# Performance work log

Measured on AMD Instinct MI355X. Metric: run time of the kernel, lower is better.

## Reference

```python
import jax, jax.numpy as jnp
import numpy as np

N_PAIRS = 100000
N_TRIP = 500000
PAIR_DIM = 128
GEOM_DIM = 4


def _mlp(x, w1, b1, w2, b2):
    return jax.nn.silu(x @ w1 + b1) @ w2 + b2


def setup_inputs() -> dict:
    key = jax.random.key(0)
    ks = jax.random.split(key, 16)

    def lin(k, fan_in, fan_out):
        bound = 1.0 / np.sqrt(fan_in)
        kw, kb = jax.random.split(k)
        w = jax.random.uniform(kw, (fan_in, fan_out), jnp.float32, -bound, bound)
        b = jax.random.uniform(kb, (fan_out,), jnp.float32, -bound, bound)
        return w, b

    psi_w1, psi_b1 = lin(ks[0], 3 * PAIR_DIM + GEOM_DIM, PAIR_DIM)
    psi_w2, psi_b2 = lin(ks[1], PAIR_DIM, PAIR_DIM)
    phi_w1, phi_b1 = lin(ks[2], 2 * PAIR_DIM, PAIR_DIM)
    phi_w2, phi_b2 = lin(ks[3], PAIR_DIM, PAIR_DIM)

    return {
        "h_pair": jax.random.normal(ks[4], (N_PAIRS, PAIR_DIM), jnp.float32),
        "pair_vu_idx": jax.random.randint(ks[5], (N_TRIP,), 0, N_PAIRS, jnp.int64 if jax.config.jax_enable_x64 else jnp.int32).astype(jnp.int32),
        "pair_uw_idx": jax.random.randint(ks[6], (N_TRIP,), 0, N_PAIRS).astype(jnp.int32),
        "pair_vw_idx": jax.random.randint(ks[7], (N_TRIP,), 0, N_PAIRS).astype(jnp.int32),
        "geom_features": jax.random.normal(ks[8], (N_TRIP, GEOM_DIM), jnp.float32),
        "psi_w1": psi_w1, "psi_b1": psi_b1, "psi_w2": psi_w2, "psi_b2": psi_b2,
        "phi_w1": phi_w1, "phi_b1": phi_b1, "phi_w2": phi_w2, "phi_b2": phi_b2,
    }


def reference(h_pair, pair_vu_idx, pair_uw_idx, pair_vw_idx, geom_features,
              psi_w1, psi_b1, psi_w2, psi_b2,
              phi_w1, phi_b1, phi_w2, phi_b2):
    # gather triplet endpoints: [T, pair_dim] each
    h_vu = h_pair[pair_vu_idx]
    h_uw = h_pair[pair_uw_idx]
    h_vw = h_pair[pair_vw_idx]
    triplet_input = jnp.concatenate([h_vu, h_uw, h_vw, geom_features], axis=-1)  # [T, 3D+G]
    m_triplet = _mlp(triplet_input, psi_w1, psi_b1, psi_w2, psi_b2)  # [T, D]
    # scatter-add back onto pairs indexed by vw
    agg = jax.ops.segment_sum(m_triplet, pair_vw_idx, num_segments=h_pair.shape[0])  # [N, D]
    updated = _mlp(jnp.concatenate([h_pair, agg], axis=-1), phi_w1, phi_b1, phi_w2, phi_b2)
    return h_pair + updated
```

## Files before the change

kernel.cpp:

```cpp
#include <hip/hip_runtime.h>
#include <hip/hip_bf16.h>

#define T_TRIP 500000
#define NP     100000
#define NTILES 7813
#define NPAD   500032

typedef float f32x4 __attribute__((ext_vector_type(4)));
typedef __bf16 bf16x8 __attribute__((ext_vector_type(8)));
typedef unsigned short u16;
typedef unsigned short u16x8 __attribute__((ext_vector_type(8)));
typedef unsigned int u32;

__device__ __forceinline__ u16 f2bf(float f) {
  union { float f; unsigned u; } v; v.f = f;
  unsigned r = v.u + 0x7fffu + ((v.u >> 16) & 1u);
  return (u16)(r >> 16);
}

__device__ __forceinline__ ushort4 cvt4(float4 v) {
  ushort4 o; o.x = f2bf(v.x); o.y = f2bf(v.y); o.z = f2bf(v.z); o.w = f2bf(v.w);
  return o;
}

__device__ __forceinline__ u16 cvt1_pk(float v) {
  unsigned r;
  asm("v_cvt_pk_bf16_f32 %0, %1, %1" : "=v"(r) : "v"(v));
  return (u16)r;
}

__device__ __forceinline__ float bflo(u32 d) {
  union { u32 u; float f; } v; v.u = d << 16; return v.f;
}
__device__ __forceinline__ float bfhi(u32 d) {
  union { u32 u; float f; } v; v.u = d & 0xffff0000u; return v.f;
}

#define MFMA16(a, b, c) __builtin_amdgcn_mfma_f32_16x16x32_bf16((a), (b), (c), 0, 0, 0)

#define WAITVM(N) asm volatile("s_waitcnt vmcnt(" #N ")" ::: "memory")
#define LGKM0()   asm volatile("s_waitcnt lgkmcnt(0)" ::: "memory")

__device__ __forceinline__ void barrier_raw() {
  asm volatile("" ::: "memory");
  __builtin_amdgcn_s_barrier();
  asm volatile("" ::: "memory");
  __builtin_amdgcn_sched_barrier(0);
}

__device__ __forceinline__ void gload_lds16(const u16* g, u16* l) {
  __builtin_amdgcn_global_load_lds((const __attribute__((address_space(1))) void*)g,
                                   (__attribute__((address_space(3))) void*)l, 16, 0, 0);
}
__device__ __forceinline__ void gload_lds4(const int* g, int* l) {
  __builtin_amdgcn_global_load_lds((const __attribute__((address_space(1))) void*)g,
                                   (__attribute__((address_space(3))) void*)l, 4, 0, 0);
}

#define FP_W1A   0u
#define FP_W1B   16384u
#define FP_W1C   32768u
#define FP_W2    49152u
#define FP_PW1   65536u
#define FP_PW2   98304u
#define FP_W1D   114688u
#define FP_H     131072u
#define FP_AGG   12931072u
#define SB_CNT2    51462144ull
#define SB_CURSOR2 51862144ull
#define SB_BSUM2   52262144ull
#define SB_TRIP    52262656ull
#define WS_S2      60263168ull

#define HSTR   136
#define HSTR2  132
#define GSTR   520
#define X2STR  264

__global__ void k_pre(const float* __restrict__ psi_w1, const float* __restrict__ psi_w2,
                      const float* __restrict__ phi_w1, const float* __restrict__ phi_w2,
                      const float* __restrict__ h, const int* __restrict__ ivw,
                      u16* __restrict__ ws, int* __restrict__ cnt) {
  const int b = blockIdx.x;
  if (b < 450) {
    int i = b * 256 + threadIdx.x;
    if (i < 49152) {
      int s = i / 16384, r = i % 16384;
      int n = r / 128, k = r % 128;
      ws[FP_W1A + i] = f2bf(psi_w1[(s * 128 + k) * 128 + n]);
      return;
    }
    i -= 49152;
    if (i < 16384) {
      int n = i / 128, k = i % 128;
      ws[FP_W2 + i] = f2bf(psi_w2[k * 128 + n]);
      return;
    }
    i -= 16384;
    if (i < 32768) {
      int n = i / 256, k = i % 256;
      ws[FP_PW1 + i] = f2bf(phi_w1[k * 128 + n]);
      return;
    }
    i -= 32768;
    if (i < 16384) {
      int n = i / 128, k = i % 128;
      ws[FP_PW2 + i] = f2bf(phi_w2[k * 128 + n]);
      return;
    }
    i -= 16384;
    if (i < 512) {
      int k = i / 128, n = i % 128;
      reinterpret_cast<float*>(ws + FP_W1D)[i] = psi_w1[(384 + k) * 128 + n];
    }
  } else if (b < 6700) {
    const size_t i = (size_t)((b - 450) * 256 + threadIdx.x) * 8;
    float4 v0 = *reinterpret_cast<const float4*>(h + i);
    float4 v1 = *reinterpret_cast<const float4*>(h + i + 4);
    *reinterpret_cast<ushort4*>(ws + FP_H + i)     = cvt4(v0);
    *reinterpret_cast<ushort4*>(ws + FP_H + i + 4) = cvt4(v1);
    ushort4 z = {0, 0, 0, 0};
    *reinterpret_cast<ushort4*>(ws + FP_AGG + i)     = z;
    *reinterpret_cast<ushort4*>(ws + FP_AGG + i + 4) = z;
  } else {
    int i = (b - 6700) * 256 + threadIdx.x;
    if (i < T_TRIP) atomicAdd(&cnt[ivw[i]], 1);
  }
}

__global__ __launch_bounds__(1024) void k_scan1(const int* __restrict__ cnt,
                                                int* __restrict__ cursor, int* __restrict__ bsum) {
  __shared__ int wsum[16];
  const int idx = blockIdx.x * 1024 + threadIdx.x;
  const int lane = threadIdx.x & 63, wid = threadIdx.x >> 6;
  int v = (idx < NP) ? cnt[idx] : 0;
  int x = v;
#pragma unroll
  for (int off = 1; off < 64; off <<= 1) {
    int n = __shfl_up(x, off);
    if (lane >= off) x += n;
  }
  if (lane == 63) wsum[wid] = x;
  __syncthreads();
  if (threadIdx.x < 16) {
    int s = wsum[threadIdx.x];
#pragma unroll
    for (int off = 1; off < 16; off <<= 1) {
      int n = __shfl_up(s, off);
      if (threadIdx.x >= off) s += n;
    }
    wsum[threadIdx.x] = s;
  }
  __syncthreads();
  const int base = wid ? wsum[wid - 1] : 0;
  if (idx < NP) cursor[idx] = base + x - v;
  if (threadIdx.x == 1023) bsum[blockIdx.x] = base + x;
}

__global__ void k_scan2(int* __restrict__ bsum) {
  __shared__ int s[128];
  const int t = threadIdx.x;
  int v = (t < 98) ? bsum[t] : 0;
  s[t] = v; __syncthreads();
#pragma unroll
  for (int off = 1; off < 128; off <<= 1) {
    int a = (t >= off) ? s[t - off] : 0;
    __syncthreads();
    s[t] += a;
    __syncthreads();
  }
  if (t < 98) bsum[t] = s[t] - v;
}

__global__ void k_scan3(const int* __restrict__ bsum, int* __restrict__ cursor) {
  int idx = blockIdx.x * 256 + threadIdx.x;
  if (idx < NP) cursor[idx] += bsum[idx >> 10];
}

__global__ void k_perm_pack(const int* __restrict__ ivu, const int* __restrict__ iuw,
                            const int* __restrict__ ivw, const float* __restrict__ geom,
                            int* __restrict__ cursor, int4* __restrict__ trip) {
  int i = blockIdx.x * 256 + threadIdx.x;
  if (i < T_TRIP) {
    int v = ivw[i];
    int pos = atomicAdd(&cursor[v], 1);
    float4 g = reinterpret_cast<const float4*>(geom)[i];
    u32 pk0, pk1;
    asm("v_cvt_pk_bf16_f32 %0, %1, %2" : "=v"(pk0) : "v"(g.x), "v"(g.y));
    asm("v_cvt_pk_bf16_f32 %0, %1, %2" : "=v"(pk1) : "v"(g.z), "v"(g.w));
    int4 rec;
    rec.x = ivu[i] | ((v & 0x7fff) << 17);
    rec.y = iuw[i] | ((v >> 15) << 17);
    rec.z = (int)pk0;
    rec.w = (int)pk1;
    trip[pos] = rec;
  } else if (i < NPAD) {
    int4 z = {0, 0, 0, 0};
    trip[i] = z;
  }
}

__global__ __launch_bounds__(256, 3) void k_triplet_sortagg(
    const u16* __restrict__ H, const int* __restrict__ trip,
    const u16* __restrict__ W1A, const u16* __restrict__ W1B, const u16* __restrict__ W1C,
    const float* __restrict__ w1dF, const u16* __restrict__ W2T,
    const float* __restrict__ b1, const float* __restrict__ b2,
    u16* __restrict__ AGG) {
  __shared__ __align__(16) u16 XB[2][16 * GSTR];
  __shared__ __align__(16) u16 hl[64 * HSTR2];
  __shared__ __align__(16) int aosT[2][256];

  u32* mlu = reinterpret_cast<u32*>(hl);

  const int tid = threadIdx.x;
  const int w = tid >> 6, l = tid & 63;
  const int lr = l & 15;
  const int lk = (l >> 4) << 3;
  const int n0 = w * 32 + lr;
  const int rowh = (l >> 4) << 2;
  const int srow = l >> 4;
  const int schunk = (l & 15) ^ ((l >> 4) << 1);

  bf16x8 w2f[4][2];
#pragma unroll
  for (int ks = 0; ks < 4; ++ks)
#pragma unroll
    for (int ct = 0; ct < 2; ++ct)
      w2f[ks][ct] = *reinterpret_cast<const bf16x8*>(&W2T[(size_t)(n0 + ct * 16) * 128 + ks * 32 + lk]);
  const float b1v[2] = {b1[n0], b1[n0 + 16]};
  const float b2v[2] = {b2[n0], b2[n0 + 16]};
  float w1dv[4][2];
#pragma unroll
  for (int k = 0; k < 4; ++k) {
    w1dv[k][0] = w1dF[k * 128 + n0];
    w1dv[k][1] = w1dF[k * 128 + n0 + 16];
  }

  auto get_idx = [&](int cb, int r, int sel) -> int {
    if (sel == 0) return aosT[cb][r * 4] & 0x1FFFF;
    if (sel == 1) return aosT[cb][r * 4 + 1] & 0x1FFFF;
    u32 d0 = (u32)aosT[cb][r * 4], d1 = (u32)aosT[cb][r * 4 + 1];
    return (int)((d0 >> 17) | ((d1 >> 17) << 15));
  };

  auto stage_src = [&](int cb, int sel, int buf) {
#pragma unroll
    for (int q = 0; q < 4; ++q) {
      const int g = w * 4 + q;
      const int idx = get_idx(cb, g * 4 + srow, sel);
      gload_lds16(H + (size_t)idx * 128 + schunk * 8, &XB[buf][g * GSTR]);
    }
  };

  auto stage_aos = [&](int tile, int cb) {
    const int* src = trip + (size_t)tile * 256;
    gload_lds4(src + w * 64 + l, &aosT[cb][w * 64]);
  };

  auto gemm_src = [&](const u16* WT, int buf, f32x4 (&acc)[4][2]) {
#pragma unroll
    for (int ks = 0; ks < 4; ++ks) {
      bf16x8 a[4], b[2];
#pragma unroll
      for (int rt = 0; rt < 4; ++rt) {
        const int r = rt * 16 + lr;
        const int g = r >> 2, s = r & 3;
        const int j = ks * 4 + (l >> 4);
        a[rt] = *reinterpret_cast<const bf16x8*>(&XB[buf][g * GSTR + s * 128 + ((j ^ (s << 1)) << 3)]);
      }
#pragma unroll
      for (int ct = 0; ct < 2; ++ct)
        b[ct] = *reinterpret_cast<const bf16x8*>(&WT[(size_t)(n0 + ct * 16) * 128 + ks * 32 + lk]);
#pragma unroll
      for (int rt = 0; rt < 4; ++rt)
#pragma unroll
        for (int ct = 0; ct < 2; ++ct)
          acc[rt][ct] = MFMA16(a[rt], b[ct], acc[rt][ct]);
    }
  };

  int cur = 0, pb = 0;
  int tt = blockIdx.x;
  const int G = gridDim.x;

  {
    int t1 = tt + G; if (t1 >= NTILES) t1 = NTILES - 1;
    stage_aos(tt, 0);
    stage_aos(t1, 1);
    WAITVM(0);
    barrier_raw();
    stage_src(0, 0 , 0);
  }

  for (; tt < NTILES; tt += G) {
    const int t0 = tt * 64;

    stage_src(cur, 1 , pb ^ 1);
    WAITVM(4);
    barrier_raw();

    f32x4 acc[4][2] = {};
    gemm_src(W1A, pb, acc);
    barrier_raw();

    stage_src(cur, 2 , pb);
    WAITVM(4);
    barrier_raw();

    gemm_src(W1B, pb ^ 1, acc);
    WAITVM(0);
    barrier_raw();

    stage_src(cur ^ 1, 0 , pb ^ 1);
    gemm_src(W1C, pb, acc);

#pragma unroll
    for (int rt = 0; rt < 4; ++rt)
#pragma unroll
      for (int j = 0; j < 4; ++j) {
        const int row = rt * 16 + rowh + j;
        const u32 d2 = (u32)aosT[cur][row * 4 + 2];
        const u32 d3 = (u32)aosT[cur][row * 4 + 3];
        const float gx = bflo(d2), gy = bfhi(d2), gz = bflo(d3), gw = bfhi(d3);
#pragma unroll
        for (int ct = 0; ct < 2; ++ct)
          acc[rt][ct][j] += gx * w1dv[0][ct] + gy * w1dv[1][ct] +
                            gz * w1dv[2][ct] + gw * w1dv[3][ct];
      }
#pragma unroll
    for (int rt = 0; rt < 4; ++rt)
#pragma unroll
      for (int ct = 0; ct < 2; ++ct) {
        const float bb = b1v[ct];
#pragma unroll
        for (int j = 0; j < 4; ++j) {
          float v = acc[rt][ct][j] + bb;
          v = v * __builtin_amdgcn_rcpf(1.f + __expf(-v));
          hl[(rt * 16 + rowh + j) * HSTR2 + n0 + ct * 16] = cvt1_pk(v);
        }
      }
    LGKM0();
    barrier_raw();

    f32x4 acc2[4][2] = {};
#pragma unroll
    for (int ks = 0; ks < 4; ++ks) {
      bf16x8 a[4];
#pragma unroll
      for (int rt = 0; rt < 4; ++rt)
        a[rt] = *reinterpret_cast<const bf16x8*>(&hl[(rt * 16 + lr) * HSTR2 + ks * 32 + lk]);
#pragma unroll
      for (int rt = 0; rt < 4; ++rt)
#pragma unroll
        for (int ct = 0; ct < 2; ++ct)
          acc2[rt][ct] = MFMA16(a[rt], w2f[ks][ct], acc2[rt][ct]);
    }
    barrier_raw();

#pragma unroll
    for (int rt = 0; rt < 4; ++rt)
#pragma unroll
      for (int j = 0; j < 4; ++j) {
        const int row = rt * 16 + rowh + j;
        float v0 = acc2[rt][0][j] + b2v[0];
        float v1 = acc2[rt][1][j] + b2v[1];
        float x0 = __shfl_xor(v0, 1);
        float x1 = __shfl_xor(v1, 1);
        const bool even = (l & 1) == 0;
        float lo = even ? v0 : x1;
        float hi = even ? x0 : v1;
        const int dcol = even ? (n0 >> 1) : ((n0 + 15) >> 1);
        u32 pk;
        asm("v_cvt_pk_bf16_f32 %0, %1, %2" : "=v"(pk) : "v"(lo), "v"(hi));
        mlu[row * 66 + dcol] = pk;
      }
    LGKM0();
    barrier_raw();

    {
      auto get_vw = [&](int r) -> int {
        u32 d0 = (u32)aosT[cur][r * 4], d1 = (u32)aosT[cur][r * 4 + 1];
        return (int)((d0 >> 17) | ((d1 >> 17) << 15));
      };
      float lo = 0.f, hi = 0.f;
      int vwc = get_vw(w * 16);
#pragma unroll 1
      for (int r8 = 0; r8 < 16; ++r8) {
        const int row = w * 16 + r8;
        const u32 d = mlu[row * 66 + l];
        if (t0 + row < T_TRIP) { lo += bflo(d); hi += bfhi(d); }
        const int vwn = (row < 63) ? get_vw(row + 1) : -1;
        if ((r8 == 15) || (vwn != vwc)) {
          u16* p = AGG + (size_t)vwc * 128 + l * 2;
          u32 pk;
          asm("v_cvt_pk_bf16_f32 %0, %1, %2" : "=v"(pk) : "v"(lo), "v"(hi));
          asm volatile("global_atomic_pk_add_bf16 %0, %1, off" :: "v"(p), "v"(pk) : "memory");
          lo = 0.f; hi = 0.f; vwc = vwn;
        }
      }
    }
    barrier_raw();

    {
      int t2 = tt + 2 * G; if (t2 >= NTILES) t2 = NTILES - 1;
      stage_aos(t2, cur);
    }

    WAITVM(0);
    barrier_raw();
    pb ^= 1; cur ^= 1;
  }
  WAITVM(0);
}

__global__ __launch_bounds__(256, 3) void k_pair_fast(
    const float* __restrict__ h_pair, const u16* __restrict__ H, const u16* __restrict__ AGG,
    const u16* __restrict__ PW1T, const u16* __restrict__ PW2T,
    const float* __restrict__ b1, const float* __restrict__ b2,
    float* __restrict__ out) {
  __shared__ __align__(16) u16 xl[64 * X2STR];
  __shared__ __align__(16) u16 hl[64 * HSTR];

  const int tid = threadIdx.x;
  const int r0 = blockIdx.x * 64;

  {
    const int row = tid >> 2, q = tid & 3;
    int rc = r0 + row; rc = (rc < NP) ? rc : (NP - 1);
    const u16x8* sh = reinterpret_cast<const u16x8*>(H + (size_t)rc * 128 + q * 32);
    const u16x8* sa = reinterpret_cast<const u16x8*>(AGG + (size_t)rc * 128 + q * 32);
    u16x8* d1 = reinterpret_cast<u16x8*>(&xl[row * X2STR + q * 32]);
    u16x8* d2 = reinterpret_cast<u16x8*>(&xl[row * X2STR + 128 + q * 32]);
#pragma unroll
    for (int i = 0; i < 4; ++i) { d1[i] = sh[i]; d2[i] = sa[i]; }
  }
  __syncthreads();

  const int w = tid >> 6, l = tid & 63;
  const int lr = l & 15;
  const int lk = (l >> 4) << 3;
  const int n0 = w * 32 + lr;
  const int rowh = (l >> 4) << 2;

  f32x4 acc[4][2] = {};
#pragma unroll 1
  for (int ks = 0; ks < 8; ++ks) {
    const int k0 = ks * 32;
    bf16x8 a[4], b[2];
#pragma unroll
    for (int rt = 0; rt < 4; ++rt)
      a[rt] = *reinterpret_cast<const bf16x8*>(&xl[(rt * 16 + lr) * X2STR + k0 + lk]);
#pragma unroll
    for (int ct = 0; ct < 2; ++ct)
      b[ct] = *reinterpret_cast<const bf16x8*>(&PW1T[(size_t)(n0 + ct * 16) * 256 + k0 + lk]);
#pragma unroll
    for (int rt = 0; rt < 4; ++rt)
#pragma unroll
      for (int ct = 0; ct < 2; ++ct)
        acc[rt][ct] = MFMA16(a[rt], b[ct], acc[rt][ct]);
  }

  {
    const float b1v0 = b1[n0], b1v1 = b1[n0 + 16];
#pragma unroll
    for (int rt = 0; rt < 4; ++rt)
#pragma unroll
      for (int ct = 0; ct < 2; ++ct) {
        const float bb = ct ? b1v1 : b1v0;
#pragma unroll
        for (int j = 0; j < 4; ++j) {
          float v = acc[rt][ct][j] + bb;
          v = v * __builtin_amdgcn_rcpf(1.f + __expf(-v));
          hl[(rt * 16 + rowh + j) * HSTR + n0 + ct * 16] = cvt1_pk(v);
        }
      }
  }
  __syncthreads();

  f32x4 acc2[4][2] = {};
#pragma unroll
  for (int ks = 0; ks < 4; ++ks) {
    const int k0 = ks * 32;
    bf16x8 a[4], b[2];
#pragma unroll
    for (int rt = 0; rt < 4; ++rt)
      a[rt] = *reinterpret_cast<const bf16x8*>(&hl[(rt * 16 + lr) * HSTR + k0 + lk]);
#pragma unroll
    for (int ct = 0; ct < 2; ++ct)
      b[ct] = *reinterpret_cast<const bf16x8*>(&PW2T[(size_t)(n0 + ct * 16) * 128 + k0 + lk]);
#pragma unroll
    for (int rt = 0; rt < 4; ++rt)
#pragma unroll
      for (int ct = 0; ct < 2; ++ct)
        acc2[rt][ct] = MFMA16(a[rt], b[ct], acc2[rt][ct]);
  }

  {
    const float b2v0 = b2[n0], b2v1 = b2[n0 + 16];
#pragma unroll
    for (int rt = 0; rt < 4; ++rt)
#pragma unroll
      for (int j = 0; j < 4; ++j) {
        const int row = rt * 16 + rowh + j;
        const int r = r0 + row;
        if (r < NP) {
          out[(size_t)r * 128 + n0]      = h_pair[(size_t)r * 128 + n0]      + acc2[rt][0][j] + b2v0;
          out[(size_t)r * 128 + n0 + 16] = h_pair[(size_t)r * 128 + n0 + 16] + acc2[rt][1][j] + b2v1;
        }
      }
  }
}

#define PSI_W1T_OFF 0
#define PSI_W2T_OFF 53248
#define PHI_W1T_OFF 69632
#define PHI_W2T_OFF 102400
#define WS_U16_TOTAL 118784
#define XSTR 424

__global__ void k_prep(const float* __restrict__ psi_w1, const float* __restrict__ psi_w2,
                       const float* __restrict__ phi_w1, const float* __restrict__ phi_w2,
                       u16* __restrict__ ws) {
  int i = blockIdx.x * 256 + threadIdx.x;
  if (i < 128 * 416) {
    int n = i / 416, k = i % 416;
    ws[PSI_W1T_OFF + i] = f2bf(k < 388 ? psi_w1[k * 128 + n] : 0.f);
    return;
  }
  i -= 128 * 416;
  if (i < 128 * 128) {
    int n = i / 128, k = i % 128;
    ws[PSI_W2T_OFF + i] = f2bf(psi_w2[k * 128 + n]);
    return;
  }
  i -= 128 * 128;
  if (i < 128 * 256) {
    int n = i / 256, k = i % 256;
    ws[PHI_W1T_OFF + i] = f2bf(phi_w1[k * 128 + n]);
    return;
  }
  i -= 128 * 256;
  if (i < 128 * 128) {
    int n = i / 128, k = i % 128;
    ws[PHI_W2T_OFF + i] = f2bf(phi_w2[k * 128 + n]);
  }
}

__global__ __launch_bounds__(256, 2) void k_triplet(
    const float* __restrict__ h_pair,
    const int* __restrict__ ivu, const int* __restrict__ iuw, const int* __restrict__ ivw,
    const float* __restrict__ geom,
    const u16* __restrict__ W1T, const u16* __restrict__ W2T,
    const float* __restrict__ b1, const float* __restrict__ b2,
    float* __restrict__ agg) {
  __shared__ __align__(16) u16 xl[64 * XSTR];
  __shared__ __align__(16) u16 hl[64 * HSTR];
  __shared__ int svw[64];

  const int tid = threadIdx.x;
  const int t0 = blockIdx.x * 64;

  {
    const int row = tid >> 2, q = tid & 3;
    const int t = t0 + row;
    const int tc = (t < T_TRIP) ? t : (T_TRIP - 1);
    if (q == 0) svw[row] = (t < T_TRIP) ? ivw[tc] : -1;
    int idx[3];
    idx[0] = ivu[tc]; idx[1] = iuw[tc]; idx[2] = ivw[tc];
#pragma unroll
    for (int s = 0; s < 3; ++s) {
      const float4* src = reinterpret_cast<const float4*>(h_pair + (size_t)idx[s] * 128 + q * 32);
      u16* dst = &xl[row * XSTR + s * 128 + q * 32];
#pragma unroll
      for (int i = 0; i < 8; ++i)
        *reinterpret_cast<ushort4*>(dst + i * 4) = cvt4(src[i]);
    }
  }
  if (tid < 64) {
    const int t = t0 + tid;
    const int tc = (t < T_TRIP) ? t : (T_TRIP - 1);
    const float4 g = reinterpret_cast<const float4*>(geom)[tc];
    u16* dst = &xl[tid * XSTR + 384];
    *reinterpret_cast<ushort4*>(dst) = cvt4(g);
    ushort4 z = {0, 0, 0, 0};
#pragma unroll
    for (int i = 1; i < 8; ++i) *reinterpret_cast<ushort4*>(dst + i * 4) = z;
  }
  __syncthreads();

  const int w = tid >> 6;
  const int l = tid & 63;
  const int lr = l & 15;
  const int lk = (l >> 4) << 3;
  const int n0 = w * 32 + lr;
  const int rowh = (l >> 4) << 2;

  f32x4 acc[4][2] = {};
#pragma unroll 1
  for (int ks = 0; ks < 13; ++ks) {
    const int k0 = ks * 32;
    bf16x8 a[4], b[2];
#pragma unroll
    for (int rt = 0; rt < 4; ++rt)
      a[rt] = *reinterpret_cast<const bf16x8*>(&xl[(rt * 16 + lr) * XSTR + k0 + lk]);
#pragma unroll
    for (int ct = 0; ct < 2; ++ct)
      b[ct] = *reinterpret_cast<const bf16x8*>(&W1T[(size_t)(n0 + ct * 16) * 416 + k0 + lk]);
#pragma unroll
    for (int rt = 0; rt < 4; ++rt)
#pragma unroll
      for (int ct = 0; ct < 2; ++ct)
        acc[rt][ct] = MFMA16(a[rt], b[ct], acc[rt][ct]);
  }

  {
    const float b1v0 = b1[n0], b1v1 = b1[n0 + 16];
#pragma unroll
    for (int rt = 0; rt < 4; ++rt)
#pragma unroll
      for (int ct = 0; ct < 2; ++ct) {
        const float bb = ct ? b1v1 : b1v0;
#pragma unroll
        for (int j = 0; j < 4; ++j) {
          float v = acc[rt][ct][j] + bb;
          v = v / (1.f + __expf(-v));
          hl[(rt * 16 + rowh + j) * HSTR + n0 + ct * 16] = f2bf(v);
        }
      }
  }
  __syncthreads();

  f32x4 acc2[4][2] = {};
#pragma unroll
  for (int ks = 0; ks < 4; ++ks) {
    const int k0 = ks * 32;
    bf16x8 a[4], b[2];
#pragma unroll
    for (int rt = 0; rt < 4; ++rt)
      a[rt] = *reinterpret_cast<const bf16x8*>(&hl[(rt * 16 + lr) * HSTR + k0 + lk]);
#pragma unroll
    for (int ct = 0; ct < 2; ++ct)
      b[ct] = *reinterpret_cast<const bf16x8*>(&W2T[(size_t)(n0 + ct * 16) * 128 + k0 + lk]);
#pragma unroll
    for (int rt = 0; rt < 4; ++rt)
#pragma unroll
      for (int ct = 0; ct < 2; ++ct)
        acc2[rt][ct] = MFMA16(a[rt], b[ct], acc2[rt][ct]);
  }

  {
    const float b2v0 = b2[n0], b2v1 = b2[n0 + 16];
#pragma unroll
    for (int rt = 0; rt < 4; ++rt)
#pragma unroll
      for (int j = 0; j < 4; ++j) {
        const int row = rt * 16 + rowh + j;
        const int dst = svw[row];
        if (dst >= 0) {
          unsafeAtomicAdd(&agg[(size_t)dst * 128 + n0], acc2[rt][0][j] + b2v0);
          unsafeAtomicAdd(&agg[(size_t)dst * 128 + n0 + 16], acc2[rt][1][j] + b2v1);
        }
      }
  }
}

__global__ __launch_bounds__(256, 2) void k_pair(
    const float* __restrict__ h_pair,
    const u16* __restrict__ W1T, const u16* __restrict__ W2T,
    const float* __restrict__ b1, const float* __restrict__ b2,
    float* __restrict__ out) {
  __shared__ __align__(16) u16 xl[64 * X2STR];
  __shared__ __align__(16) u16 hl[64 * HSTR];

  const int tid = threadIdx.x;
  const int r0 = blockIdx.x * 64;

  {
    const int row = tid >> 2, q = tid & 3;
    const int r = r0 + row;
    const int rc = (r < NP) ? r : (NP - 1);
    const float4* s1 = reinterpret_cast<const float4*>(h_pair + (size_t)rc * 128 + q * 32);
    const float4* s2 = reinterpret_cast<const float4*>(out + (size_t)rc * 128 + q * 32);
    u16* d1 = &xl[row * X2STR + q * 32];
    u16* d2 = &xl[row * X2STR + 128 + q * 32];
#pragma unroll
    for (int i = 0; i < 8; ++i) {
      *reinterpret_cast<ushort4*>(d1 + i * 4) = cvt4(s1[i]);
      *reinterpret_cast<ushort4*>(d2 + i * 4) = cvt4(s2[i]);
    }
  }
  __syncthreads();

  const int w = tid >> 6;
  const int l = tid & 63;
  const int lr = l & 15;
  const int lk = (l >> 4) << 3;
  const int n0 = w * 32 + lr;
  const int rowh = (l >> 4) << 2;

  f32x4 acc[4][2] = {};
#pragma unroll 1
  for (int ks = 0; ks < 8; ++ks) {
    const int k0 = ks * 32;
    bf16x8 a[4], b[2];
#pragma unroll
    for (int rt = 0; rt < 4; ++rt)
      a[rt] = *reinterpret_cast<const bf16x8*>(&xl[(rt * 16 + lr) * X2STR + k0 + lk]);
#pragma unroll
    for (int ct = 0; ct < 2; ++ct)
      b[ct] = *reinterpret_cast<const bf16x8*>(&W1T[(size_t)(n0 + ct * 16) * 256 + k0 + lk]);
#pragma unroll
    for (int rt = 0; rt < 4; ++rt)
#pragma unroll
      for (int ct = 0; ct < 2; ++ct)
        acc[rt][ct] = MFMA16(a[rt], b[ct], acc[rt][ct]);
  }

  {
    const float b1v0 = b1[n0], b1v1 = b1[n0 + 16];
#pragma unroll
    for (int rt = 0; rt < 4; ++rt)
#pragma unroll
      for (int ct = 0; ct < 2; ++ct) {
        const float bb = ct ? b1v1 : b1v0;
#pragma unroll
        for (int j = 0; j < 4; ++j) {
          float v = acc[rt][ct][j] + bb;
          v = v / (1.f + __expf(-v));
          hl[(rt * 16 + rowh + j) * HSTR + n0 + ct * 16] = f2bf(v);
        }
      }
  }
  __syncthreads();

  f32x4 acc2[4][2] = {};
#pragma unroll
  for (int ks = 0; ks < 4; ++ks) {
    const int k0 = ks * 32;
    bf16x8 a[4], b[2];
#pragma unroll
    for (int rt = 0; rt < 4; ++rt)
      a[rt] = *reinterpret_cast<const bf16x8*>(&hl[(rt * 16 + lr) * HSTR + k0 + lk]);
#pragma unroll
    for (int ct = 0; ct < 2; ++ct)
      b[ct] = *reinterpret_cast<const bf16x8*>(&W2T[(size_t)(n0 + ct * 16) * 128 + k0 + lk]);
#pragma unroll
    for (int rt = 0; rt < 4; ++rt)
#pragma unroll
      for (int ct = 0; ct < 2; ++ct)
        acc2[rt][ct] = MFMA16(a[rt], b[ct], acc2[rt][ct]);
  }

  {
    const float b2v0 = b2[n0], b2v1 = b2[n0 + 16];
#pragma unroll
    for (int rt = 0; rt < 4; ++rt)
#pragma unroll
      for (int j = 0; j < 4; ++j) {
        const int row = rt * 16 + rowh + j;
        const int r = r0 + row;
        if (r < NP) {
          out[(size_t)r * 128 + n0]      = h_pair[(size_t)r * 128 + n0]      + acc2[rt][0][j] + b2v0;
          out[(size_t)r * 128 + n0 + 16] = h_pair[(size_t)r * 128 + n0 + 16] + acc2[rt][1][j] + b2v1;
        }
      }
  }
}

extern "C" void kernel_launch(void* const* d_in, const int* in_sizes, int n_in,
                              void* d_out, int out_size, void* d_ws, size_t ws_size,
                              hipStream_t stream) {
  const float* h_pair = (const float*)d_in[0];
  const int* ivu = (const int*)d_in[1];
  const int* iuw = (const int*)d_in[2];
  const int* ivw = (const int*)d_in[3];
  const float* geom = (const float*)d_in[4];
  const float* psi_w1 = (const float*)d_in[5];
  const float* psi_b1 = (const float*)d_in[6];
  const float* psi_w2 = (const float*)d_in[7];
  const float* psi_b2 = (const float*)d_in[8];
  const float* phi_w1 = (const float*)d_in[9];
  const float* phi_b1 = (const float*)d_in[10];
  const float* phi_w2 = (const float*)d_in[11];
  const float* phi_b2 = (const float*)d_in[12];

  float* out = (float*)d_out;
  u16* ws = (u16*)d_ws;
  char* wsb = (char*)d_ws;

  if (ws_size >= WS_S2) {
    int*  cnt    = (int*)(wsb + SB_CNT2);
    int*  cursor = (int*)(wsb + SB_CURSOR2);
    int*  bsum   = (int*)(wsb + SB_BSUM2);
    int4* trip   = (int4*)(wsb + SB_TRIP);

    hipMemsetAsync(cnt, 0, NP * sizeof(int), stream);
    k_pre<<<8654, 256, 0, stream>>>(psi_w1, psi_w2, phi_w1, phi_w2, h_pair, ivw, ws, cnt);
    k_scan1<<<98, 1024, 0, stream>>>(cnt, cursor, bsum);
    k_scan2<<<1, 128, 0, stream>>>(bsum);
    k_scan3<<<391, 256, 0, stream>>>(bsum, cursor);
    k_perm_pack<<<(NPAD + 255) / 256, 256, 0, stream>>>(ivu, iuw, ivw, geom, cursor, trip);
    k_triplet_sortagg<<<768, 256, 0, stream>>>(
        ws + FP_H, (const int*)trip,
        ws + FP_W1A, ws + FP_W1B, ws + FP_W1C,
        reinterpret_cast<const float*>(ws + FP_W1D), ws + FP_W2,
        psi_b1, psi_b2, ws + FP_AGG);
    k_pair_fast<<<(NP + 63) / 64, 256, 0, stream>>>(
        h_pair, ws + FP_H, ws + FP_AGG,
        ws + FP_PW1, ws + FP_PW2, phi_b1, phi_b2, out);
  } else {
    hipMemsetAsync(d_out, 0, (size_t)out_size * sizeof(float), stream);
    k_prep<<<(WS_U16_TOTAL + 255) / 256, 256, 0, stream>>>(psi_w1, psi_w2, phi_w1, phi_w2, ws);
    k_triplet<<<(T_TRIP + 63) / 64, 256, 0, stream>>>(
        h_pair, ivu, iuw, ivw, geom,
        ws + PSI_W1T_OFF, ws + PSI_W2T_OFF, psi_b1, psi_b2, out);
    k_pair<<<(NP + 63) / 64, 256, 0, stream>>>(
        h_pair, ws + PHI_W1T_OFF, ws + PHI_W2T_OFF, phi_b1, phi_b2, out);
  }
}
```

Before: 286.6 us.

## Stage all three gathered sources at once and fold scan3 into perm_pack

Removes the k_scan3 launch by adding the block prefix offset directly inside k_perm_pack's atomic cursor. In the triplet kernel, the double-buffered interleave of staging and GEMM is replaced by a triple LDS buffer: all three gathered sources are loaded, followed by one wait and one barrier, and then three back-to-back GEMMs. Occupancy drops from 3 to 2 blocks per SM with a 512-block grid, and the segmented reduce preloads its rows and indices into registers and is fully unrolled. This cuts barriers and launch overhead but loses the overlap of the gather with MFMA work and adds register pressure.

```diff
diff --git a/kernel.cpp b/kernel.cpp
--- a/kernel.cpp
+++ b/kernel.cpp
@@ -172,18 +172,14 @@
   if (t < 98) bsum[t] = s[t] - v;
 }
 
-__global__ void k_scan3(const int* __restrict__ bsum, int* __restrict__ cursor) {
-  int idx = blockIdx.x * 256 + threadIdx.x;
-  if (idx < NP) cursor[idx] += bsum[idx >> 10];
-}
-
 __global__ void k_perm_pack(const int* __restrict__ ivu, const int* __restrict__ iuw,
                             const int* __restrict__ ivw, const float* __restrict__ geom,
-                            int* __restrict__ cursor, int4* __restrict__ trip) {
+                            int* __restrict__ cursor, const int* __restrict__ bsum,
+                            int4* __restrict__ trip) {
   int i = blockIdx.x * 256 + threadIdx.x;
   if (i < T_TRIP) {
     int v = ivw[i];
-    int pos = atomicAdd(&cursor[v], 1);
+    int pos = atomicAdd(&cursor[v], 1) + bsum[v >> 10];
     float4 g = reinterpret_cast<const float4*>(geom)[i];
     u32 pk0, pk1;
     asm("v_cvt_pk_bf16_f32 %0, %1, %2" : "=v"(pk0) : "v"(g.x), "v"(g.y));
@@ -200,13 +196,13 @@
   }
 }
 
-__global__ __launch_bounds__(256, 3) void k_triplet_sortagg(
+__global__ __launch_bounds__(256, 2) void k_triplet_sortagg(
     const u16* __restrict__ H, const int* __restrict__ trip,
     const u16* __restrict__ W1A, const u16* __restrict__ W1B, const u16* __restrict__ W1C,
     const float* __restrict__ w1dF, const u16* __restrict__ W2T,
     const float* __restrict__ b1, const float* __restrict__ b2,
     u16* __restrict__ AGG) {
-  __shared__ __align__(16) u16 XB[2][16 * GSTR];
+  __shared__ __align__(16) u16 XB[3][16 * GSTR];
   __shared__ __align__(16) u16 hl[64 * HSTR2];
   __shared__ __align__(16) int aosT[2][256];
 
@@ -279,7 +275,7 @@
     }
   };
 
-  int cur = 0, pb = 0;
+  int cur = 0;
   int tt = blockIdx.x;
   const int G = gridDim.x;
 
@@ -289,30 +285,21 @@
     stage_aos(t1, 1);
     WAITVM(0);
     barrier_raw();
-    stage_src(0, 0 , 0);
   }
 
   for (; tt < NTILES; tt += G) {
     const int t0 = tt * 64;
 
-    stage_src(cur, 1 , pb ^ 1);
-    WAITVM(4);
-    barrier_raw();
-
-    f32x4 acc[4][2] = {};
-    gemm_src(W1A, pb, acc);
-    barrier_raw();
-
-    stage_src(cur, 2 , pb);
-    WAITVM(4);
-    barrier_raw();
-
-    gemm_src(W1B, pb ^ 1, acc);
+    stage_src(cur, 0, 0);
+    stage_src(cur, 1, 1);
+    stage_src(cur, 2, 2);
     WAITVM(0);
     barrier_raw();
 
-    stage_src(cur ^ 1, 0 , pb ^ 1);
-    gemm_src(W1C, pb, acc);
+    f32x4 acc[4][2] = {};
+    gemm_src(W1A, 0, acc);
+    gemm_src(W1B, 1, acc);
+    gemm_src(W1C, 2, acc);
 
 #pragma unroll
     for (int rt = 0; rt < 4; ++rt)
@@ -378,24 +365,34 @@
     barrier_raw();
 
     {
-      auto get_vw = [&](int r) -> int {
-        u32 d0 = (u32)aosT[cur][r * 4], d1 = (u32)aosT[cur][r * 4 + 1];
-        return (int)((d0 >> 17) | ((d1 >> 17) << 15));
-      };
+      u32 md[16];
+#pragma unroll
+      for (int r8 = 0; r8 < 16; ++r8)
+        md[r8] = mlu[(w * 16 + r8) * 66 + l];
+      int vws[16];
+#pragma unroll
+      for (int r8 = 0; r8 < 16; ++r8) {
+        const int r = w * 16 + r8;
+        const u32 d0 = (u32)aosT[cur][r * 4], d1 = (u32)aosT[cur][r * 4 + 1];
+        vws[r8] = (int)((d0 >> 17) | ((d1 >> 17) << 15));
+      }
       float lo = 0.f, hi = 0.f;
-      int vwc = get_vw(w * 16);
-#pragma unroll 1
+#pragma unroll
       for (int r8 = 0; r8 < 16; ++r8) {
         const int row = w * 16 + r8;
-        const u32 d = mlu[row * 66 + l];
-        if (t0 + row < T_TRIP) { lo += bflo(d); hi += bfhi(d); }
-        const int vwn = (row < 63) ? get_vw(row + 1) : -1;
-        if ((r8 == 15) || (vwn != vwc)) {
-          u16* p = AGG + (size_t)vwc * 128 + l * 2;
+        if (t0 + row < T_TRIP) { lo += bflo(md[r8]); hi += bfhi(md[r8]); }
+        const bool flush = (r8 == 15) || (vws[(r8 + 1) & 15] != vws[r8] || r8 == 15);
+        if ((r8 == 15) || (vws[r8 + 1 > 15 ? 15 : r8 + 1] != vws[r8]) || flush == false) {
+        }
+        bool doflush;
+        if (r8 == 15) doflush = true;
+        else doflush = (vws[r8 + 1] != vws[r8]);
+        if (doflush) {
+          u16* p = AGG + (size_t)vws[r8] * 128 + l * 2;
           u32 pk;
           asm("v_cvt_pk_bf16_f32 %0, %1, %2" : "=v"(pk) : "v"(lo), "v"(hi));
           asm volatile("global_atomic_pk_add_bf16 %0, %1, off" :: "v"(p), "v"(pk) : "memory");
-          lo = 0.f; hi = 0.f; vwc = vwn;
+          lo = 0.f; hi = 0.f;
         }
       }
     }
@@ -408,7 +405,7 @@
 
     WAITVM(0);
     barrier_raw();
-    pb ^= 1; cur ^= 1;
+    cur ^= 1;
   }
   WAITVM(0);
 }
@@ -798,9 +795,8 @@
     k_pre<<<8654, 256, 0, stream>>>(psi_w1, psi_w2, phi_w1, phi_w2, h_pair, ivw, ws, cnt);
     k_scan1<<<98, 1024, 0, stream>>>(cnt, cursor, bsum);
     k_scan2<<<1, 128, 0, stream>>>(bsum);
-    k_scan3<<<391, 256, 0, stream>>>(bsum, cursor);
-    k_perm_pack<<<(NPAD + 255) / 256, 256, 0, stream>>>(ivu, iuw, ivw, geom, cursor, trip);
-    k_triplet_sortagg<<<768, 256, 0, stream>>>(
+    k_perm_pack<<<(NPAD + 255) / 256, 256, 0, stream>>>(ivu, iuw, ivw, geom, cursor, bsum, trip);
+    k_triplet_sortagg<<<512, 256, 0, stream>>>(
         ws + FP_H, (const int*)trip,
         ws + FP_W1A, ws + FP_W1B, ws + FP_W1C,
         reinterpret_cast<const float*>(ws + FP_W1D), ws + FP_W2,
```

Measured after the change: 295.4 us. 3.1% more time.
